# Performance work log

Measured on AMD Instinct MI355X. Metric: run time of the kernel, lower is better.

## Reference

```python
import jax, jax.numpy as jnp
import numpy as np

K = 3  # filter_size
PAD = (K - 1) // 2


def setup_inputs() -> dict:
    key = jax.random.key(0)
    k1, k2, k3 = jax.random.split(key, 3)
    B, C, H, Wd = 4, 256, 128, 128
    x = jax.random.normal(k1, (B, C, H, Wd), dtype=jnp.float32)
    # 1x1 conv params: out_channels = C * K^2
    W = jax.random.normal(k2, (C * K * K, C), dtype=jnp.float32) * (1.0 / np.sqrt(C))
    b = jax.random.normal(k3, (C * K * K,), dtype=jnp.float32) * 0.01
    return {"x": x, "W": W, "b": b}


def _extract_patches(x):
    # x: (B,C,H,W) -> (B,C,H,W,K*K), kernel positions row-major (matches F.unfold)
    B, C, H, Wd = x.shape
    xp = jnp.pad(x, ((0, 0), (0, 0), (PAD, PAD), (PAD, PAD)))
    patches = jnp.stack(
        [xp[:, :, i:i + H, j:j + Wd] for i in range(K) for j in range(K)],
        axis=-1,
    )
    return patches


def reference(x, W, b):
    B, C, H, Wd = x.shape
    # 1x1 conv: (B,C,H,W) x (C*K^2, C) -> (B, C*K^2, H, W)
    filters = jnp.einsum('bchw,oc->bohw', x, W) + b[None, :, None, None]
    # view(B, C, K^2, H, W) then permute to (B,C,H,W,K^2)
    filters = filters.reshape(B, C, K * K, H, Wd).transpose(0, 1, 3, 4, 2)
    patches = _extract_patches(x)  # (B,C,H,W,K^2), unfold ordering c-major then pos
    return jnp.sum(patches * filters, axis=-1)  # (B,C,H,W)
```

## Files before the change

kernel.cpp:

```cpp
#include <hip/hip_runtime.h>


typedef __attribute__((ext_vector_type(8))) short bf16x8;
typedef __attribute__((ext_vector_type(4))) float f32x4;

__device__ __forceinline__ unsigned int f2bf(float f) {
    unsigned int u = __float_as_uint(f);
    return (u + 0x7fffu + ((u >> 16) & 1u)) >> 16;
}
__device__ __forceinline__ unsigned int pack2(float a, float b) {
    return f2bf(a) | (f2bf(b) << 16);
}

__global__ __launch_bounds__(256) void wconv_kernel(const float* __restrict__ W,
                                                    unsigned char* __restrict__ Wb) {
    int idx0 = blockIdx.x * 256 + threadIdx.x;
    int o = idx0 >> 5, g = idx0 & 31;
    const float4* src = (const float4*)(W + ((size_t)o << 8) + ((size_t)g << 3));
    float4 v0 = src[0], v1 = src[1];
    uint4 pk;
    pk.x = pack2(v0.x, v0.y); pk.y = pack2(v0.z, v0.w);
    pk.z = pack2(v1.x, v1.y); pk.w = pack2(v1.z, v1.w);
    int kh = g >> 4, g2 = g & 15, s = g2 >> 2, kq = g2 & 3;
    int chunk = o / 144, oc = o - chunk * 144;
    int c_local = oc / 9, p = oc - c_local * 9;
    int q = c_local >> 2, c4 = c_local & 3;
    int idx = c4 * 9 + p;
    int ni = idx >> 2, j = idx & 3, r = (q << 2) + j;
    int jsub = kh * 3 + ni / 3, ni_ = ni % 3;
    size_t dst = (size_t)chunk * 73728 + (size_t)jsub * 12288
               + (size_t)(s * 3 + ni_) * 1024 + (size_t)((kq << 4) + r) * 16;
    *(uint4*)(Wb + dst) = pk;
}


#define SYNC_VM(N) asm volatile("s_waitcnt vmcnt(" #N ") lgkmcnt(0)\n\ts_barrier" ::: "memory")
#define SYNC_LG    asm volatile("s_waitcnt lgkmcnt(0)\n\ts_barrier" ::: "memory")
#define FENCE      asm volatile("" ::: "memory")

#define STAGE(CH, J)                                                            \
    do {                                                                        \
        const int sl_ = (wv < 6) ? wv : (wv - 6);                               \
        const unsigned char* bs_ = Wb + (size_t)(CH) * 73728                    \
            + (size_t)(J) * 12288 + sl_ * 2048 + (lane << 4);                   \
        unsigned char* bd_ = smem + ((J) % 4) * 12288 + sl_ * 2048;             \
        __builtin_amdgcn_global_load_lds(                                       \
            (const __attribute__((address_space(1))) void*)(bs_),               \
            (__attribute__((address_space(3))) void*)(bd_), 16, 0, 0);          \
        __builtin_amdgcn_global_load_lds(                                       \
            (const __attribute__((address_space(1))) void*)(bs_ + 1024),        \
            (__attribute__((address_space(3))) void*)(bd_ + 1024), 16, 0, 0);   \
    } while (0)

#define MFMA_SUB(J)                                                             \
    do {                                                                        \
        const int kh_ = (J) / 3, snib_ = ((J) % 3) * 3;                         \
        const unsigned char* bb_ = smem + ((J) % 4) * 12288 + (lane << 4);      \
        _Pragma("unroll")                                                       \
        for (int s_ = 0; s_ < 4; ++s_) {                                        \
            const bf16x8 a0_ = afr[(kh_ << 2) + s_];                            \
            const bf16x8 a1_ = afr[8 + (kh_ << 2) + s_];                        \
            _Pragma("unroll")                                                   \
            for (int ni_ = 0; ni_ < 3; ++ni_) {                                 \
                const bf16x8 bq_ = *(const bf16x8*)(bb_ + ((s_ * 3 + ni_) << 10)); \
                acc[0][snib_ + ni_] = __builtin_amdgcn_mfma_f32_16x16x32_bf16(  \
                    bq_, a0_, acc[0][snib_ + ni_], 0, 0, 0);                    \
                acc[1][snib_ + ni_] = __builtin_amdgcn_mfma_f32_16x16x32_bf16(  \
                    bq_, a1_, acc[1][snib_ + ni_], 0, 0, 0);                    \
            }                                                                   \
        }                                                                       \
    } while (0)

__global__ __launch_bounds__(512, 2) void dfgemm_kernel(
        const unsigned char* __restrict__ Wb, const float* __restrict__ x,
        const float* __restrict__ bias, float* __restrict__ out) {
    __shared__ __align__(16) unsigned char smem[49152];

    const int t = threadIdx.x;
    const int lane = t & 63, wv = t >> 6;
    const int quad = lane >> 4, lrow = lane & 15;

    const int b = blockIdx.x >> 6;
    const int hp = blockIdx.x & 63;
    const int h = (hp << 1) + (wv >> 2);
    const int wq = wv & 3;

    STAGE(0, 0); STAGE(0, 1); STAGE(0, 2); STAGE(0, 3);

    bf16x8 afr[16];
    {
        const float* xrow = x + ((size_t)b << 22) + (h << 7);
        #pragma unroll
        for (int mi = 0; mi < 2; ++mi) {
            const int w = (wq << 5) + (mi << 4) + lrow;
            #pragma unroll
            for (int gg = 0; gg < 8; ++gg) {
                const float* p = xrow + ((size_t)((gg << 5) + (quad << 3)) << 14) + w;
                float v[8];
                #pragma unroll
                for (int e = 0; e < 8; ++e) v[e] = p[(size_t)e << 14];
                uint4 pk;
                pk.x = pack2(v[0], v[1]); pk.y = pack2(v[2], v[3]);
                pk.z = pack2(v[4], v[5]); pk.w = pack2(v[6], v[7]);
                afr[(mi << 3) + gg] = *(const bf16x8*)&pk;
            }
        }
    }
    SYNC_VM(0);

    #pragma unroll 1
    for (int chunk = 0; chunk < 16; ++chunk) {
        const int c1 = (chunk + 1) & 15;
        f32x4 acc[2][9];
        const f32x4 zero = {0.f, 0.f, 0.f, 0.f};
        #pragma unroll
        for (int mi = 0; mi < 2; ++mi)
            #pragma unroll
            for (int ni = 0; ni < 9; ++ni) acc[mi][ni] = zero;

        SYNC_VM(8);
        MFMA_SUB(0);

        SYNC_VM(8);
        STAGE(chunk, 4);
        MFMA_SUB(1);

        SYNC_VM(8);
        STAGE(chunk, 5);
        MFMA_SUB(2);

        SYNC_VM(8);
        STAGE(c1, 2);
        MFMA_SUB(3);

        SYNC_VM(4);
        STAGE(c1, 3);
        MFMA_SUB(4);

        SYNC_VM(4);
        STAGE(c1, 0);
        MFMA_SUB(5);

        SYNC_LG;
        STAGE(c1, 1);
        FENCE;

        #pragma unroll
        for (int mi = 0; mi < 2; ++mi) {
            const int w = (wq << 5) + (mi << 4) + lrow;
            #pragma unroll
            for (int c4 = 0; c4 < 4; ++c4) {
                const int cg = (chunk << 4) + (quad << 2) + c4;
                const float* bp = bias + cg * 9;
                const float* xc = x + ((size_t)((b << 8) + cg) << 14);
                float sum = 0.f;
                #pragma unroll
                for (int p = 0; p < 9; ++p) {
                    const int idx = c4 * 9 + p;
                    const int ni = idx >> 2, j = idx & 3;
                    const float yv = acc[mi][ni][j];
                    const int hh = h + p / 3 - 1, ww = w + p % 3 - 1;
                    float xv = 0.f;
                    if ((unsigned)hh < 128u && (unsigned)ww < 128u)
                        xv = xc[(hh << 7) + ww];
                    sum += (yv + bp[p]) * xv;
                }
                out[((size_t)((b << 8) + cg) << 14) + (h << 7) + w] = sum;
            }
        }
    }
}

extern "C" void kernel_launch(void* const* d_in, const int* in_sizes, int n_in,
                              void* d_out, int out_size, void* d_ws, size_t ws_size,
                              hipStream_t stream) {
    const float* x    = (const float*)d_in[0];
    const float* W    = (const float*)d_in[1];
    const float* bias = (const float*)d_in[2];
    float* out = (float*)d_out;

    unsigned char* Wb = (unsigned char*)d_ws;

    wconv_kernel<<<288, 256, 0, stream>>>(W, Wb);
    dfgemm_kernel<<<256, 512, 0, stream>>>(Wb, x, bias, out);
}
```

Measured before the change: 213.8 us.

## Halve per-wave M tile to one row per block, doubling grid and occupancy

Each block now covers a single image row with 8 waves each owning 16 pixels, instead of two rows with each wave owning 32 pixels. The A-fragment and accumulator register arrays shrink by half, launch bounds request 4 blocks per CU, and the grid doubles to 512 blocks. The aim is to raise occupancy and fill more CUs, trading away B-tile reuse so each staged weight tile in LDS feeds half as many MFMAs and the weights are streamed twice as often overall.

```diff
diff --git a/kernel.cpp b/kernel.cpp
--- a/kernel.cpp
+++ b/kernel.cpp
@@ -58,20 +58,17 @@
         const unsigned char* bb_ = smem + ((J) % 4) * 12288 + (lane << 4);      \
         _Pragma("unroll")                                                       \
         for (int s_ = 0; s_ < 4; ++s_) {                                        \
-            const bf16x8 a0_ = afr[(kh_ << 2) + s_];                            \
-            const bf16x8 a1_ = afr[8 + (kh_ << 2) + s_];                        \
+            const bf16x8 a_ = afr[(kh_ << 2) + s_];                             \
             _Pragma("unroll")                                                   \
             for (int ni_ = 0; ni_ < 3; ++ni_) {                                 \
                 const bf16x8 bq_ = *(const bf16x8*)(bb_ + ((s_ * 3 + ni_) << 10)); \
-                acc[0][snib_ + ni_] = __builtin_amdgcn_mfma_f32_16x16x32_bf16(  \
-                    bq_, a0_, acc[0][snib_ + ni_], 0, 0, 0);                    \
-                acc[1][snib_ + ni_] = __builtin_amdgcn_mfma_f32_16x16x32_bf16(  \
-                    bq_, a1_, acc[1][snib_ + ni_], 0, 0, 0);                    \
+                acc[snib_ + ni_] = __builtin_amdgcn_mfma_f32_16x16x32_bf16(     \
+                    bq_, a_, acc[snib_ + ni_], 0, 0, 0);                        \
             }                                                                   \
         }                                                                       \
     } while (0)
 
-__global__ __launch_bounds__(512, 2) void dfgemm_kernel(
+__global__ __launch_bounds__(512, 4) void dfgemm_kernel(
         const unsigned char* __restrict__ Wb, const float* __restrict__ x,
         const float* __restrict__ bias, float* __restrict__ out) {
     __shared__ __align__(16) unsigned char smem[49152];
@@ -80,30 +77,25 @@
     const int lane = t & 63, wv = t >> 6;
     const int quad = lane >> 4, lrow = lane & 15;
 
-    const int b = blockIdx.x >> 6;
-    const int hp = blockIdx.x & 63;
-    const int h = (hp << 1) + (wv >> 2);
-    const int wq = wv & 3;
+    const int b = blockIdx.x >> 7;
+    const int h = blockIdx.x & 127;
+    const int w = (wv << 4) + lrow;
 
     STAGE(0, 0); STAGE(0, 1); STAGE(0, 2); STAGE(0, 3);
 
-    bf16x8 afr[16];
+    bf16x8 afr[8];
     {
         const float* xrow = x + ((size_t)b << 22) + (h << 7);
         #pragma unroll
-        for (int mi = 0; mi < 2; ++mi) {
-            const int w = (wq << 5) + (mi << 4) + lrow;
+        for (int gg = 0; gg < 8; ++gg) {
+            const float* p = xrow + ((size_t)((gg << 5) + (quad << 3)) << 14) + w;
+            float v[8];
             #pragma unroll
-            for (int gg = 0; gg < 8; ++gg) {
-                const float* p = xrow + ((size_t)((gg << 5) + (quad << 3)) << 14) + w;
-                float v[8];
-                #pragma unroll
-                for (int e = 0; e < 8; ++e) v[e] = p[(size_t)e << 14];
-                uint4 pk;
-                pk.x = pack2(v[0], v[1]); pk.y = pack2(v[2], v[3]);
-                pk.z = pack2(v[4], v[5]); pk.w = pack2(v[6], v[7]);
-                afr[(mi << 3) + gg] = *(const bf16x8*)&pk;
-            }
+            for (int e = 0; e < 8; ++e) v[e] = p[(size_t)e << 14];
+            uint4 pk;
+            pk.x = pack2(v[0], v[1]); pk.y = pack2(v[2], v[3]);
+            pk.z = pack2(v[4], v[5]); pk.w = pack2(v[6], v[7]);
+            afr[gg] = *(const bf16x8*)&pk;
         }
     }
     SYNC_VM(0);
@@ -111,12 +103,10 @@
     #pragma unroll 1
     for (int chunk = 0; chunk < 16; ++chunk) {
         const int c1 = (chunk + 1) & 15;
-        f32x4 acc[2][9];
+        f32x4 acc[9];
         const f32x4 zero = {0.f, 0.f, 0.f, 0.f};
         #pragma unroll
-        for (int mi = 0; mi < 2; ++mi)
-            #pragma unroll
-            for (int ni = 0; ni < 9; ++ni) acc[mi][ni] = zero;
+        for (int ni = 0; ni < 9; ++ni) acc[ni] = zero;
 
         SYNC_VM(8);
         MFMA_SUB(0);
@@ -146,27 +136,23 @@
         FENCE;
 
         #pragma unroll
-        for (int mi = 0; mi < 2; ++mi) {
-            const int w = (wq << 5) + (mi << 4) + lrow;
+        for (int c4 = 0; c4 < 4; ++c4) {
+            const int cg = (chunk << 4) + (quad << 2) + c4;
+            const float* bp = bias + cg * 9;
+            const float* xc = x + ((size_t)((b << 8) + cg) << 14);
+            float sum = 0.f;
             #pragma unroll
-            for (int c4 = 0; c4 < 4; ++c4) {
-                const int cg = (chunk << 4) + (quad << 2) + c4;
-                const float* bp = bias + cg * 9;
-                const float* xc = x + ((size_t)((b << 8) + cg) << 14);
-                float sum = 0.f;
-                #pragma unroll
-                for (int p = 0; p < 9; ++p) {
-                    const int idx = c4 * 9 + p;
-                    const int ni = idx >> 2, j = idx & 3;
-                    const float yv = acc[mi][ni][j];
-                    const int hh = h + p / 3 - 1, ww = w + p % 3 - 1;
-                    float xv = 0.f;
-                    if ((unsigned)hh < 128u && (unsigned)ww < 128u)
-                        xv = xc[(hh << 7) + ww];
-                    sum += (yv + bp[p]) * xv;
-                }
-                out[((size_t)((b << 8) + cg) << 14) + (h << 7) + w] = sum;
+            for (int p = 0; p < 9; ++p) {
+                const int idx = c4 * 9 + p;
+                const int ni = idx >> 2, j = idx & 3;
+                const float yv = acc[ni][j];
+                const int hh = h + p / 3 - 1, ww = w + p % 3 - 1;
+                float xv = 0.f;
+                if ((unsigned)hh < 128u && (unsigned)ww < 128u)
+                    xv = xc[(hh << 7) + ww];
+                sum += (yv + bp[p]) * xv;
             }
+            out[((size_t)((b << 8) + cg) << 14) + (h << 7) + w] = sum;
         }
     }
 }
@@ -182,5 +168,5 @@
     unsigned char* Wb = (unsigned char*)d_ws;
 
     wconv_kernel<<<288, 256, 0, stream>>>(W, Wb);
-    dfgemm_kernel<<<256, 512, 0, stream>>>(Wb, x, bias, out);
+    dfgemm_kernel<<<512, 512, 0, stream>>>(Wb, x, bias, out);
 }
```

Result: faster. 206.1 us (-3.6%).

## Use one row per 4-wave block with a full six-slot LDS weight buffer

Applied to the files above, without the earlier changes.

Each block now covers a single output row with 4 waves instead of two rows with 8 waves, which doubles the grid to 512 blocks of 256 threads. The weight staging buffer grows from a 4-slot ring of 48KB to all 6 sub-tiles (72KB), and each wave issues 3 async global-to-LDS loads per stage. The loop prefetches the whole next chunk slot by slot, with wait counts adjusted to match. The aim is fewer LDS-slot reuse stalls and simpler prefetch. In exchange, each weight chunk is now fetched once per row rather than once per row pair, and fewer waves are resident per CU.

```diff
diff --git a/kernel.cpp b/kernel.cpp
--- a/kernel.cpp
+++ b/kernel.cpp
@@ -40,22 +40,20 @@
 
 #define STAGE(CH, J)                                                            \
     do {                                                                        \
-        const int sl_ = (wv < 6) ? wv : (wv - 6);                               \
         const unsigned char* bs_ = Wb + (size_t)(CH) * 73728                    \
-            + (size_t)(J) * 12288 + sl_ * 2048 + (lane << 4);                   \
-        unsigned char* bd_ = smem + ((J) % 4) * 12288 + sl_ * 2048;             \
-        __builtin_amdgcn_global_load_lds(                                       \
-            (const __attribute__((address_space(1))) void*)(bs_),               \
-            (__attribute__((address_space(3))) void*)(bd_), 16, 0, 0);          \
-        __builtin_amdgcn_global_load_lds(                                       \
-            (const __attribute__((address_space(1))) void*)(bs_ + 1024),        \
-            (__attribute__((address_space(3))) void*)(bd_ + 1024), 16, 0, 0);   \
+            + (size_t)(J) * 12288 + wv * 3072 + (lane << 4);                    \
+        unsigned char* bd_ = smem + (size_t)(J) * 12288 + wv * 3072;            \
+        _Pragma("unroll")                                                       \
+        for (int c_ = 0; c_ < 3; ++c_)                                          \
+            __builtin_amdgcn_global_load_lds(                                   \
+                (const __attribute__((address_space(1))) void*)(bs_ + c_ * 1024), \
+                (__attribute__((address_space(3))) void*)(bd_ + c_ * 1024), 16, 0, 0); \
     } while (0)
 
 #define MFMA_SUB(J)                                                             \
     do {                                                                        \
         const int kh_ = (J) / 3, snib_ = ((J) % 3) * 3;                         \
-        const unsigned char* bb_ = smem + ((J) % 4) * 12288 + (lane << 4);      \
+        const unsigned char* bb_ = smem + (size_t)(J) * 12288 + (lane << 4);    \
         _Pragma("unroll")                                                       \
         for (int s_ = 0; s_ < 4; ++s_) {                                        \
             const bf16x8 a0_ = afr[(kh_ << 2) + s_];                            \
@@ -71,28 +69,27 @@
         }                                                                       \
     } while (0)
 
-__global__ __launch_bounds__(512, 2) void dfgemm_kernel(
+__global__ __launch_bounds__(256, 2) void dfgemm_kernel(
         const unsigned char* __restrict__ Wb, const float* __restrict__ x,
         const float* __restrict__ bias, float* __restrict__ out) {
-    __shared__ __align__(16) unsigned char smem[49152];
+    __shared__ __align__(16) unsigned char smem[73728];
 
     const int t = threadIdx.x;
     const int lane = t & 63, wv = t >> 6;
     const int quad = lane >> 4, lrow = lane & 15;
 
-    const int b = blockIdx.x >> 6;
-    const int hp = blockIdx.x & 63;
-    const int h = (hp << 1) + (wv >> 2);
-    const int wq = wv & 3;
+    const int b = blockIdx.x >> 7;
+    const int h = blockIdx.x & 127;
 
-    STAGE(0, 0); STAGE(0, 1); STAGE(0, 2); STAGE(0, 3);
+    STAGE(0, 0); STAGE(0, 1); STAGE(0, 2);
+    STAGE(0, 3); STAGE(0, 4); STAGE(0, 5);
 
     bf16x8 afr[16];
     {
         const float* xrow = x + ((size_t)b << 22) + (h << 7);
         #pragma unroll
         for (int mi = 0; mi < 2; ++mi) {
-            const int w = (wq << 5) + (mi << 4) + lrow;
+            const int w = (wv << 5) + (mi << 4) + lrow;
             #pragma unroll
             for (int gg = 0; gg < 8; ++gg) {
                 const float* p = xrow + ((size_t)((gg << 5) + (quad << 3)) << 14) + w;
@@ -122,32 +119,32 @@
         MFMA_SUB(0);
 
         SYNC_VM(8);
-        STAGE(chunk, 4);
+        STAGE(c1, 0);
         MFMA_SUB(1);
 
-        SYNC_VM(8);
-        STAGE(chunk, 5);
+        SYNC_VM(11);
+        STAGE(c1, 1);
         MFMA_SUB(2);
 
-        SYNC_VM(8);
+        SYNC_VM(14);
         STAGE(c1, 2);
         MFMA_SUB(3);
 
-        SYNC_VM(4);
+        SYNC_VM(17);
         STAGE(c1, 3);
         MFMA_SUB(4);
 
-        SYNC_VM(4);
-        STAGE(c1, 0);
+        SYNC_VM(20);
+        STAGE(c1, 4);
         MFMA_SUB(5);
 
         SYNC_LG;
-        STAGE(c1, 1);
+        STAGE(c1, 5);
         FENCE;
 
         #pragma unroll
         for (int mi = 0; mi < 2; ++mi) {
-            const int w = (wq << 5) + (mi << 4) + lrow;
+            const int w = (wv << 5) + (mi << 4) + lrow;
             #pragma unroll
             for (int c4 = 0; c4 < 4; ++c4) {
                 const int cg = (chunk << 4) + (quad << 2) + c4;
@@ -182,5 +179,5 @@
     unsigned char* Wb = (unsigned char*)d_ws;
 
     wconv_kernel<<<288, 256, 0, stream>>>(W, Wb);
-    dfgemm_kernel<<<256, 512, 0, stream>>>(Wb, x, bias, out);
+    dfgemm_kernel<<<512, 256, 0, stream>>>(Wb, x, bias, out);
 }
```

After: 210.2 us. About the same (-1.7%).
